# Kernel tuning notes

Measured on AMD Instinct MI355X. Metric: run time of the kernel, lower is better.

## Reference

```python
import jax, jax.numpy as jnp
import numpy as np

B, T, S = 64, 128, 16
E = 512           # d2v input size
H = 512           # bi-LSTM output size (args.d2v_embed)
Hh = H // 2       # per-direction hidden
NL = 2            # num_layers
ED = 128          # args.embedding_dim
USERS, ARTS, PAD = 100000, 100000, 0


def setup_inputs() -> dict:
    key = jax.random.key(0)
    ks = jax.random.split(key, 32)
    p = 0.02
    inp = {}
    inp["x1"] = jax.random.normal(ks[0], (B, T, E), jnp.float32)
    inp["sample_d2v_embeds"] = jax.random.normal(ks[1], (B, T, S, H), jnp.float32)
    # LSTM params: layer-0 input E == layer-1 input H, so stackable. gate order i,f,g,o
    inp["lstm_Wih"] = jax.random.normal(ks[2], (NL, 2, 4 * Hh, E), jnp.float32) * p
    inp["lstm_Whh"] = jax.random.normal(ks[3], (NL, 2, 4 * Hh, Hh), jnp.float32) * p
    inp["lstm_bih"] = jax.random.normal(ks[4], (NL, 2, 4 * Hh), jnp.float32) * p
    inp["lstm_bhh"] = jax.random.normal(ks[5], (NL, 2, 4 * Hh), jnp.float32) * p
    inp["attn_W1"] = jax.random.normal(ks[6], (H, H), jnp.float32) * p
    inp["attn_b1"] = jax.random.normal(ks[7], (H,), jnp.float32) * p
    inp["attn_w2"] = jax.random.normal(ks[8], (H,), jnp.float32) * p
    inp["rnn_mlp_W"] = jax.random.normal(ks[9], (64, H), jnp.float32) * p
    inp["rnn_mlp_b"] = jax.random.normal(ks[10], (64,), jnp.float32) * p
    inp["user_table"] = jax.random.normal(ks[11], (USERS, ED), jnp.float32) * p
    inp["art_table"] = (jax.random.normal(ks[12], (ARTS, ED), jnp.float32) * p).at[PAD].set(0.0)
    inp["em_W1"] = jax.random.normal(ks[13], (128, ED), jnp.float32) * p
    inp["em_b1"] = jax.random.normal(ks[14], (128,), jnp.float32) * p
    inp["em_W2"] = jax.random.normal(ks[15], (64, 128), jnp.float32) * p
    inp["em_b2"] = jax.random.normal(ks[16], (64,), jnp.float32) * p
    inp["lm_W1"] = jax.random.normal(ks[17], (256, 128), jnp.float32) * p
    inp["lm_b1"] = jax.random.normal(ks[18], (256,), jnp.float32) * p
    inp["lm_W2"] = jax.random.normal(ks[19], (128, 256), jnp.float32) * p
    inp["lm_b2"] = jax.random.normal(ks[20], (128,), jnp.float32) * p
    inp["lm_W3"] = jax.random.normal(ks[21], (64, 128), jnp.float32) * p
    inp["lm_b3"] = jax.random.normal(ks[22], (64,), jnp.float32) * p
    inp["lm_W4"] = jax.random.normal(ks[23], (1, 64), jnp.float32) * p
    inp["lm_b4"] = jax.random.normal(ks[24], (1,), jnp.float32) * p
    inp["x2"] = 0  # unused '_' arg
    inp["cate"] = jax.random.randint(ks[25], (B, T), 0, 10)  # unused by forward
    lens = jax.random.randint(ks[26], (B,), 1, T + 1)
    inp["seq_lens"] = jnp.sort(lens)[::-1]  # pack requires descending
    inp["user_ids"] = jax.random.randint(ks[27], (B,), 0, USERS)
    inp["sample_ids"] = jax.random.randint(ks[28], (B, T, S), 0, ARTS)
    return inp


def _bilstm(x, lens, Wih, Whh, bih, bhh):
    # Packed bidirectional LSTM == padded LSTM with state updates masked to t < len.
    Bc, Tc, _ = x.shape
    tmask = jnp.arange(Tc)[None, :] < lens[:, None]       # [B,T]
    m_t = tmask.T[:, :, None]                             # [T,B,1]
    for l in range(NL):
        outs = []
        for d, rev in ((0, False), (1, True)):
            xg = jnp.einsum('bti,gi->tbg', x, Wih[l, d]) + bih[l, d]  # [T,B,4Hh]
            Whh_ld, bhh_ld = Whh[l, d], bhh[l, d]

            def step(carry, inp_t, Whh_ld=Whh_ld, bhh_ld=bhh_ld):
                h, c = carry
                xg_t, m = inp_t
                g = xg_t + h @ Whh_ld.T + bhh_ld
                i_, f_, g_, o_ = jnp.split(g, 4, axis=-1)
                c2 = jax.nn.sigmoid(f_) * c + jax.nn.sigmoid(i_) * jnp.tanh(g_)
                h2 = jax.nn.sigmoid(o_) * jnp.tanh(c2)
                h = jnp.where(m, h2, h)
                c = jnp.where(m, c2, c)
                return (h, c), h

            init = (jnp.zeros((Bc, Hh), x.dtype), jnp.zeros((Bc, Hh), x.dtype))
            _, hs = jax.lax.scan(step, init, (xg, m_t), reverse=rev)
            outs.append(jnp.transpose(hs, (1, 0, 2)))
        x = jnp.concatenate(outs, axis=-1)                # [B,T,H]
    return x, tmask


def reference(x1, sample_d2v_embeds, lstm_Wih, lstm_Whh, lstm_bih, lstm_bhh,
              attn_W1, attn_b1, attn_w2, rnn_mlp_W, rnn_mlp_b,
              user_table, art_table, em_W1, em_b1, em_W2, em_b2,
              lm_W1, lm_b1, lm_W2, lm_b2, lm_W3, lm_b3, lm_W4, lm_b4,
              x2, cate, seq_lens, user_ids, sample_ids):
    rnn, tmask = _bilstm(x1, seq_lens, lstm_Wih, lstm_Whh, lstm_bih, lstm_bhh)
    # per-key MLP attention score, causal softmax, weighted sum (the packed double loop)
    sc = jnp.einsum('bth,h->bt', jnp.tanh(jnp.einsum('bth,oh->bto', rnn, attn_W1) + attn_b1), attn_w2)
    causal = jnp.tril(jnp.ones((rnn.shape[1], rnn.shape[1]), bool))
    logits = jnp.where(causal[None, :, :], sc[:, None, :], jnp.float32(-1e30))
    a = jax.nn.softmax(logits, axis=-1)                   # [B,T(query),T(key)]
    ctx = jnp.einsum('bts,bsh->bth', a, rnn)
    ctx = jnp.where(tmask[:, :, None], ctx, 0.0)          # rnn_step zeros at padded t
    # embedding branch
    ue = user_table[user_ids]                             # [B,ED]
    se = art_table[sample_ids]                            # [B,T,S,ED]
    e = ue[:, None, None, :] * se
    e = jax.nn.relu(e @ em_W1.T + em_b1)
    e = jax.nn.relu(e @ em_W2.T + em_b2)                  # [B,T,S,64]
    # rnn branch
    r = ctx[:, :, None, :] * sample_d2v_embeds
    r = r @ rnn_mlp_W.T + rnn_mlp_b                       # [B,T,S,64]
    z = jnp.concatenate([e, r], axis=-1)                  # [B,T,S,128]
    z = jax.nn.relu(z @ lm_W1.T + lm_b1)
    z = jax.nn.relu(z @ lm_W2.T + lm_b2)
    z = jax.nn.relu(z @ lm_W3.T + lm_b3)
    z = jax.nn.sigmoid(z @ lm_W4.T + lm_b4)
    return jnp.squeeze(z, axis=-1)                        # [B,T,S]
```

## Files before the change

kernel.cpp:

```cpp
#include <hip/hip_runtime.h>
#include <cstddef>

namespace {

constexpr int T = 128;

typedef unsigned short u16;
typedef unsigned int u32;
typedef __attribute__((ext_vector_type(8))) short short8;
typedef __attribute__((ext_vector_type(4))) float f32x4;
typedef __attribute__((ext_vector_type(4))) int i32x4;

__device__ __forceinline__ u16 f2bf(float x) {
  u32 u = __float_as_uint(x);
  u = (u + 0x7FFFu + ((u >> 16) & 1u)) >> 16;
  return (u16)u;
}
__device__ __forceinline__ float bf2f(u16 v) {
  return __uint_as_float(((u32)v) << 16);
}
__device__ __forceinline__ float sigf(float x) {
  return __builtin_amdgcn_rcpf(1.f + __builtin_amdgcn_exp2f(-1.44269504f * x));
}
__device__ __forceinline__ float tanh2(float x) {
  return 1.f - 2.f * __builtin_amdgcn_rcpf(1.f + __builtin_amdgcn_exp2f(2.88539008f * x));
}

constexpr int O_WIH = 0;
constexpr int O_AW1 = 2097152;
constexpr int O_EM1 = 2359296;
constexpr int O_EM2 = 2375680;
constexpr int O_MLP = 2383872;
constexpr int O_LW1 = 2416640;
constexpr int O_LW2 = 2449408;
constexpr int O_LW3 = 2482176;
constexpr int N_WBF = 2490368;

__global__ __launch_bounds__(256)
void k_prep(const float* __restrict__ wih, const float* __restrict__ aw1,
            const float* __restrict__ e1, const float* __restrict__ e2,
            const float* __restrict__ mw, const float* __restrict__ l1,
            const float* __restrict__ l2, const float* __restrict__ l3,
            u16* __restrict__ wbf) {
  int i = blockIdx.x * 256 + threadIdx.x;
  if (i >= N_WBF) return;
  float v;
  if (i < O_AW1)      v = wih[i];
  else if (i < O_EM1) v = aw1[i - O_AW1];
  else if (i < O_EM2) v = e1[i - O_EM1];
  else if (i < O_MLP) v = e2[i - O_EM2];
  else if (i < O_LW1) v = mw[i - O_MLP];
  else if (i < O_LW2) v = l1[i - O_LW1];
  else if (i < O_LW3) v = l2[i - O_LW2];
  else                v = l3[i - O_LW3];
  wbf[i] = f2bf(v);
}

__global__ __launch_bounds__(256)
void k_prepw(const float* __restrict__ whh, signed char* __restrict__ wq) {
  int i = blockIdx.x * 256 + threadIdx.x;
  float v = whh[i] * 1016.f;
  v = fminf(fmaxf(v, -127.f), 127.f);
  wq[i] = (signed char)(int)rintf(v);
}

__global__ __launch_bounds__(256)
void k_xg_mfma(const float* __restrict__ X, const u16* __restrict__ Wbf,
               const float* __restrict__ bi, const float* __restrict__ bh,
               float* __restrict__ xg) {
  __shared__ __align__(16) u16 sx[32 * 520];
  int tid = threadIdx.x;
  int rowbase = blockIdx.x * 32;
  int nchunk = blockIdx.y;
  for (int idx = tid; idx < 4096; idx += 256) {
    int r = idx >> 7, k4 = idx & 127;
    float4 v = *(const float4*)(X + (size_t)(rowbase + r) * 512 + k4 * 4);
    u32* p = (u32*)(sx + r * 520 + k4 * 4);
    p[0] = (u32)f2bf(v.x) | ((u32)f2bf(v.y) << 16);
    p[1] = (u32)f2bf(v.z) | ((u32)f2bf(v.w) << 16);
  }
  __syncthreads();
  int w = tid >> 6, lane = tid & 63;
  int msub = w >> 1, nhalf = w & 1;
  int mbase = msub * 16;
  int nb0 = nchunk * 256 + nhalf * 128;
  f32x4 acc[8];
#pragma unroll
  for (int i = 0; i < 8; ++i) acc[i] = f32x4{0.f, 0.f, 0.f, 0.f};
  for (int kt = 0; kt < 16; ++kt) {
    short8 a = *(const short8*)(sx + (mbase + (lane & 15)) * 520 + kt * 32 + (lane >> 4) * 8);
#pragma unroll
    for (int nt = 0; nt < 8; ++nt) {
      short8 b = *(const short8*)(Wbf + (size_t)(nb0 + nt * 16 + (lane & 15)) * 512 +
                                  kt * 32 + (lane >> 4) * 8);
      acc[nt] = __builtin_amdgcn_mfma_f32_16x16x32_bf16(a, b, acc[nt], 0, 0, 0);
    }
  }
  int mr = mbase + (lane >> 4) * 4;
#pragma unroll
  for (int nt = 0; nt < 8; ++nt) {
    int n = nb0 + nt * 16 + (lane & 15);
    float bb = bi[n] + bh[n];
#pragma unroll
    for (int r = 0; r < 4; ++r)
      xg[(size_t)(rowbase + mr + r) * 2048 + n] = acc[nt][r] + bb;
  }
}

__global__ __launch_bounds__(512, 1)
void k_lstm6(const float* __restrict__ xg, const signed char* __restrict__ wq,
             const int* __restrict__ lens, float* __restrict__ out, int layer) {
  __shared__ __align__(16) signed char hq[2][16 * 272];
  const int d = blockIdx.x >> 2, bg = blockIdx.x & 3;
  const int tid = threadIdx.x;
  const int jc = tid >> 6, l = tid & 63, ln = l & 15, lk = l >> 4;
  const int mb = bg * 16;

  i32x4 Bq[4][2][4];
  const signed char* wbase = wq + (size_t)(layer * 2 + d) * 262144;
#pragma unroll
  for (int g = 0; g < 4; ++g)
#pragma unroll
    for (int js = 0; js < 2; ++js)
#pragma unroll
      for (int kc = 0; kc < 4; ++kc) {
        int n = g * 256 + jc * 32 + js * 16 + ln;
        Bq[g][js][kc] = *(const i32x4*)(wbase + (size_t)n * 256 + kc * 64 + lk * 16);
      }

  int mlen[4];
#pragma unroll
  for (int r = 0; r < 4; ++r) mlen[r] = lens[mb + lk * 4 + r];

  float cst[2][4], hst[2][4];
#pragma unroll
  for (int js = 0; js < 2; ++js)
#pragma unroll
    for (int r = 0; r < 4; ++r) { cst[js][r] = 0.f; hst[js][r] = 0.f; }

  const float DEQ = 1.f / (1016.f * 127.f);

  for (int s = 0; s < 128; ++s) {
    const int t = d ? (127 - s) : s;

    float xv[4][2][4];
#pragma unroll
    for (int g = 0; g < 4; ++g)
#pragma unroll
      for (int js = 0; js < 2; ++js)
#pragma unroll
        for (int r = 0; r < 4; ++r)
          xv[g][js][r] = xg[((size_t)(mb + lk * 4 + r) * 128 + t) * 2048 +
                            d * 1024 + g * 256 + jc * 32 + js * 16 + ln];

    i32x4 acc[4][2];
#pragma unroll
    for (int g = 0; g < 4; ++g)
#pragma unroll
      for (int js = 0; js < 2; ++js) acc[g][js] = i32x4{0, 0, 0, 0};

    if (s > 0) {
      const signed char* hr = hq[(s & 1) ^ 1];
#pragma unroll
      for (int kc = 0; kc < 4; ++kc) {
        i32x4 a = *(const i32x4*)(hr + ln * 272 + kc * 64 + lk * 16);
#pragma unroll
        for (int g = 0; g < 4; ++g)
#pragma unroll
          for (int js = 0; js < 2; ++js)
            acc[g][js] = __builtin_amdgcn_mfma_i32_16x16x64_i8(a, Bq[g][js][kc],
                                                               acc[g][js], 0, 0, 0);
      }
    }

    signed char* hw = hq[s & 1];
#pragma unroll
    for (int js = 0; js < 2; ++js)
#pragma unroll
      for (int r = 0; r < 4; ++r) {
        float gi = (float)acc[0][js][r] * DEQ + xv[0][js][r];
        float gf = (float)acc[1][js][r] * DEQ + xv[1][js][r];
        float gg = (float)acc[2][js][r] * DEQ + xv[2][js][r];
        float go = (float)acc[3][js][r] * DEQ + xv[3][js][r];
        float c2 = sigf(gf) * cst[js][r] + sigf(gi) * tanh2(gg);
        float h2 = sigf(go) * tanh2(c2);
        const int m = lk * 4 + r;
        bool upd = t < mlen[r];
        cst[js][r] = upd ? c2 : cst[js][r];
        float hn = upd ? h2 : hst[js][r];
        hst[js][r] = hn;
        const int j = jc * 32 + js * 16 + ln;
        out[((size_t)(mb + m) * 128 + t) * 512 + d * 256 + j] = hn;
        hw[m * 272 + j] = (signed char)(int)rintf(hn * 127.f);
      }
    __syncthreads();
  }
}

__global__ __launch_bounds__(256)
void k_attn(const float* __restrict__ rnn, const u16* __restrict__ W1bf,
            const float* __restrict__ b1, const float* __restrict__ w2,
            float* __restrict__ sc) {
  __shared__ __align__(16) u16 sx[32 * 520];
  __shared__ float sred[32];
  int tid = threadIdx.x;
  int rowbase = blockIdx.x * 32;
  for (int idx = tid; idx < 4096; idx += 256) {
    int r = idx >> 7, k4 = idx & 127;
    float4 v = *(const float4*)(rnn + (size_t)(rowbase + r) * 512 + k4 * 4);
    u32* p = (u32*)(sx + r * 520 + k4 * 4);
    p[0] = (u32)f2bf(v.x) | ((u32)f2bf(v.y) << 16);
    p[1] = (u32)f2bf(v.z) | ((u32)f2bf(v.w) << 16);
  }
  if (tid < 32) sred[tid] = 0.f;
  __syncthreads();
  int w = tid >> 6, lane = tid & 63;
  int msub = w >> 1, nhalf = w & 1;
  int mbase = msub * 16;
  float psum[4] = {0.f, 0.f, 0.f, 0.f};
  for (int ng = 0; ng < 4; ++ng) {
    f32x4 acc[4];
#pragma unroll
    for (int i = 0; i < 4; ++i) acc[i] = f32x4{0.f, 0.f, 0.f, 0.f};
    for (int kt = 0; kt < 16; ++kt) {
      short8 a = *(const short8*)(sx + (mbase + (lane & 15)) * 520 + kt * 32 + (lane >> 4) * 8);
#pragma unroll
      for (int nt = 0; nt < 4; ++nt) {
        int nrow = nhalf * 256 + ng * 64 + nt * 16 + (lane & 15);
        short8 b = *(const short8*)(W1bf + (size_t)nrow * 512 + kt * 32 + (lane >> 4) * 8);
        acc[nt] = __builtin_amdgcn_mfma_f32_16x16x32_bf16(a, b, acc[nt], 0, 0, 0);
      }
    }
#pragma unroll
    for (int nt = 0; nt < 4; ++nt) {
      int n = nhalf * 256 + ng * 64 + nt * 16 + (lane & 15);
      float wn = w2[n], bn = b1[n];
#pragma unroll
      for (int r = 0; r < 4; ++r) psum[r] += wn * tanh2(acc[nt][r] + bn);
    }
  }
#pragma unroll
  for (int off = 8; off >= 1; off >>= 1)
#pragma unroll
    for (int r = 0; r < 4; ++r) psum[r] += __shfl_xor(psum[r], off);
  if ((lane & 15) == 0) {
#pragma unroll
    for (int r = 0; r < 4; ++r)
      atomicAdd(&sred[msub * 16 + (lane >> 4) * 4 + r], psum[r]);
  }
  __syncthreads();
  if (tid < 32) sc[rowbase + tid] = sred[tid];
}

__global__ __launch_bounds__(128)
void k_ctx(const float* __restrict__ sc, const float* __restrict__ rnn,
           const int* __restrict__ lens, float* __restrict__ ctx) {
  int b = blockIdx.x;
  int h = blockIdx.y * 128 + threadIdx.x;
  __shared__ float ex[T];
  ex[threadIdx.x] = expf(sc[b * T + threadIdx.x]);
  __syncthreads();
  int len = lens[b];
  float acc = 0.f, den = 0.f;
  for (int t = 0; t < T; ++t) {
    float wv = ex[t];
    den += wv;
    acc += wv * rnn[((size_t)b * T + t) * 512 + h];
    ctx[((size_t)b * T + t) * 512 + h] = (t < len) ? (acc / den) : 0.f;
  }
}

template <int NT, int KT, bool RELU>
__device__ __forceinline__ void stage_mfma(const u16* __restrict__ Wbf,
                                           const float* __restrict__ bias,
                                           const u16* A, int lda,
                                           u16* O, int ldo, int nofs,
                                           int lane, int msub, int nhalf) {
  f32x4 acc[NT];
#pragma unroll
  for (int i = 0; i < NT; ++i) acc[i] = f32x4{0.f, 0.f, 0.f, 0.f};
  int mbase = msub * 16;
  int nb0 = nhalf * (NT * 16);
#pragma unroll
  for (int kt = 0; kt < KT; ++kt) {
    short8 a = *(const short8*)(A + (mbase + (lane & 15)) * lda + kt * 32 + (lane >> 4) * 8);
#pragma unroll
    for (int nt = 0; nt < NT; ++nt) {
      short8 b = *(const short8*)(Wbf + (size_t)(nb0 + nt * 16 + (lane & 15)) * (KT * 32) +
                                  kt * 32 + (lane >> 4) * 8);
      acc[nt] = __builtin_amdgcn_mfma_f32_16x16x32_bf16(a, b, acc[nt], 0, 0, 0);
    }
  }
  int mr = mbase + (lane >> 4) * 4;
#pragma unroll
  for (int nt = 0; nt < NT; ++nt) {
    int nl = nb0 + nt * 16 + (lane & 15);
    float bv = bias[nl];
#pragma unroll
    for (int r = 0; r < 4; ++r) {
      float v = acc[nt][r] + bv;
      if (RELU) v = fmaxf(v, 0.f);
      O[(mr + r) * ldo + nofs + nl] = f2bf(v);
    }
  }
}

__global__ __launch_bounds__(256)
void k_sample(const float* __restrict__ ctx, const float* __restrict__ d2v,
              const float* __restrict__ user_table, const float* __restrict__ art_table,
              const int* __restrict__ user_ids, const int* __restrict__ sample_ids,
              const u16* __restrict__ wbf,
              const float* __restrict__ em_b1, const float* __restrict__ em_b2,
              const float* __restrict__ mlp_b,
              const float* __restrict__ lm_b1, const float* __restrict__ lm_b2,
              const float* __restrict__ lm_b3,
              const float* __restrict__ lm_W4, const float* __restrict__ lm_b4,
              float* __restrict__ out) {
  __shared__ __align__(16) u16 bufA[32 * 520];
  __shared__ __align__(16) u16 bufB[32 * 264];
  __shared__ __align__(16) u16 bufC[32 * 136];
  int tid = threadIdx.x, lane = tid & 63, w = tid >> 6;
  int msub = w >> 1, nhalf = w & 1;
  int rowbase = blockIdx.x * 32;

  for (int idx = tid; idx < 1024; idx += 256) {
    int r = idx >> 5, k4 = idx & 31;
    int m = rowbase + r;
    int sid = sample_ids[m];
    int uid = user_ids[m >> 11];
    float4 u = *(const float4*)(user_table + (size_t)uid * 128 + k4 * 4);
    float4 a = *(const float4*)(art_table + (size_t)sid * 128 + k4 * 4);
    u32* p = (u32*)(bufA + r * 520 + k4 * 4);
    p[0] = (u32)f2bf(u.x * a.x) | ((u32)f2bf(u.y * a.y) << 16);
    p[1] = (u32)f2bf(u.z * a.z) | ((u32)f2bf(u.w * a.w) << 16);
  }
  __syncthreads();
  stage_mfma<4, 4, true>(wbf + O_EM1, em_b1, bufA, 520, bufB, 264, 0, lane, msub, nhalf);
  __syncthreads();
  stage_mfma<2, 4, true>(wbf + O_EM2, em_b2, bufB, 264, bufC, 136, 0, lane, msub, nhalf);
  for (int idx = tid; idx < 4096; idx += 256) {
    int r = idx >> 7, k4 = idx & 127;
    int m = rowbase + r;
    int bt = m >> 4;
    float4 cx = *(const float4*)(ctx + (size_t)bt * 512 + k4 * 4);
    float4 dv = *(const float4*)(d2v + (size_t)m * 512 + k4 * 4);
    u32* p = (u32*)(bufA + r * 520 + k4 * 4);
    p[0] = (u32)f2bf(cx.x * dv.x) | ((u32)f2bf(cx.y * dv.y) << 16);
    p[1] = (u32)f2bf(cx.z * dv.z) | ((u32)f2bf(cx.w * dv.w) << 16);
  }
  __syncthreads();
  stage_mfma<2, 16, false>(wbf + O_MLP, mlp_b, bufA, 520, bufC, 136, 64, lane, msub, nhalf);
  __syncthreads();
  stage_mfma<8, 4, true>(wbf + O_LW1, lm_b1, bufC, 136, bufB, 264, 0, lane, msub, nhalf);
  __syncthreads();
  stage_mfma<4, 8, true>(wbf + O_LW2, lm_b2, bufB, 264, bufA, 520, 0, lane, msub, nhalf);
  __syncthreads();
  stage_mfma<2, 4, true>(wbf + O_LW3, lm_b3, bufA, 520, bufC, 136, 0, lane, msub, nhalf);
  __syncthreads();

  if (tid < 32) {
    float acc = lm_b4[0];
#pragma unroll
    for (int k = 0; k < 64; ++k) acc += bf2f(bufC[tid * 136 + k]) * lm_W4[k];
    out[rowbase + tid] = sigf(acc);
  }
}

}

extern "C" void kernel_launch(void* const* d_in, const int* in_sizes, int n_in,
                              void* d_out, int out_size, void* d_ws, size_t ws_size,
                              hipStream_t stream) {
  const float* x1   = (const float*)d_in[0];
  const float* d2v  = (const float*)d_in[1];
  const float* Wih  = (const float*)d_in[2];
  const float* Whh  = (const float*)d_in[3];
  const float* bih  = (const float*)d_in[4];
  const float* bhh  = (const float*)d_in[5];
  const float* aW1  = (const float*)d_in[6];
  const float* ab1  = (const float*)d_in[7];
  const float* aw2  = (const float*)d_in[8];
  const float* mlpW = (const float*)d_in[9];
  const float* mlpb = (const float*)d_in[10];
  const float* utab = (const float*)d_in[11];
  const float* atab = (const float*)d_in[12];
  const float* emW1 = (const float*)d_in[13];
  const float* emb1 = (const float*)d_in[14];
  const float* emW2 = (const float*)d_in[15];
  const float* emb2 = (const float*)d_in[16];
  const float* lmW1 = (const float*)d_in[17];
  const float* lmb1 = (const float*)d_in[18];
  const float* lmW2 = (const float*)d_in[19];
  const float* lmb2 = (const float*)d_in[20];
  const float* lmW3 = (const float*)d_in[21];
  const float* lmb3 = (const float*)d_in[22];
  const float* lmW4 = (const float*)d_in[23];
  const float* lmb4 = (const float*)d_in[24];
  const int* lens   = (const int*)d_in[27];
  const int* uids   = (const int*)d_in[28];
  const int* sids   = (const int*)d_in[29];
  float* out = (float*)d_out;

  float* ws = (float*)d_ws;
  signed char* WQ = (signed char*)ws;
  float* SC  = ws + 262144;
  u16* WBF = (u16*)(ws + 270336);
  float* XG  = ws + 1515520;
  float* R0  = ws + 18292736;
  float* R1  = ws + 22487040;
  float* CTX = ws + 18292736;

  k_prep<<<(N_WBF + 255) / 256, 256, 0, stream>>>(Wih, aW1, emW1, emW2, mlpW,
                                                  lmW1, lmW2, lmW3, WBF);
  k_prepw<<<4096, 256, 0, stream>>>(Whh, WQ);
  k_xg_mfma<<<dim3(256, 8), 256, 0, stream>>>(x1, WBF + O_WIH, bih, bhh, XG);
  k_lstm6<<<8, 512, 0, stream>>>(XG, WQ, lens, R0, 0);
  k_xg_mfma<<<dim3(256, 8), 256, 0, stream>>>(R0, WBF + O_WIH + 1048576,
                                              bih + 2048, bhh + 2048, XG);
  k_lstm6<<<8, 512, 0, stream>>>(XG, WQ, lens, R1, 1);
  k_attn<<<256, 256, 0, stream>>>(R1, WBF + O_AW1, ab1, aw2, SC);
  k_ctx<<<dim3(64, 4), 128, 0, stream>>>(SC, R1, lens, CTX);
  k_sample<<<4096, 256, 0, stream>>>(CTX, d2v, utab, atab, uids, sids, WBF,
                                     emb1, emb2, mlpb, lmb1, lmb2, lmb3,
                                     lmW4, lmb4, out);
}
```

Baseline: 1.267 ms.

## Halve k_sample LDS with split-K d2v staging, fuse final layers, lighter barriers

The k_sample kernel's large 520-stride buffer shrinks to 264 by staging the ctx*d2v product in two 256-wide K chunks. The rnn MLP matmul is written out by hand and accumulated across both chunks. The last two MLP layers are fused: the 64-wide ReLU output is dotted with lm_W4 in registers, reduced with shuffles and LDS atomics, so the bufC round trip and the serial 32-thread tail go away. __syncthreads is replaced with a raw lgkmcnt wait plus s_barrier, in both the LSTM loop and k_sample, to cut barrier overhead. Less LDS should allow more resident blocks, at the cost of an extra barrier and a serialized reload between the K halves.

```diff
diff --git a/kernel.cpp b/kernel.cpp
--- a/kernel.cpp
+++ b/kernel.cpp
@@ -24,6 +24,9 @@
 }
 __device__ __forceinline__ float tanh2(float x) {
   return 1.f - 2.f * __builtin_amdgcn_rcpf(1.f + __builtin_amdgcn_exp2f(2.88539008f * x));
+}
+__device__ __forceinline__ void bar_lds() {
+  asm volatile("s_waitcnt lgkmcnt(0)\n\ts_barrier" ::: "memory");
 }
 
 constexpr int O_WIH = 0;
@@ -193,7 +196,7 @@
         out[((size_t)(mb + m) * 128 + t) * 512 + d * 256 + j] = hn;
         hw[m * 272 + j] = (signed char)(int)rintf(hn * 127.f);
       }
-    __syncthreads();
+    bar_lds();
   }
 }
 
@@ -316,12 +319,16 @@
               const float* __restrict__ lm_b3,
               const float* __restrict__ lm_W4, const float* __restrict__ lm_b4,
               float* __restrict__ out) {
-  __shared__ __align__(16) u16 bufA[32 * 520];
+  __shared__ __align__(16) u16 bufA[32 * 264];
   __shared__ __align__(16) u16 bufB[32 * 264];
   __shared__ __align__(16) u16 bufC[32 * 136];
+  __shared__ float sred[32];
   int tid = threadIdx.x, lane = tid & 63, w = tid >> 6;
   int msub = w >> 1, nhalf = w & 1;
+  int mbase = msub * 16;
   int rowbase = blockIdx.x * 32;
+
+  if (tid < 32) sred[tid] = 0.f;
 
   for (int idx = tid; idx < 1024; idx += 256) {
     int r = idx >> 5, k4 = idx & 31;
@@ -330,40 +337,108 @@
     int uid = user_ids[m >> 11];
     float4 u = *(const float4*)(user_table + (size_t)uid * 128 + k4 * 4);
     float4 a = *(const float4*)(art_table + (size_t)sid * 128 + k4 * 4);
-    u32* p = (u32*)(bufA + r * 520 + k4 * 4);
+    u32* p = (u32*)(bufA + r * 264 + k4 * 4);
     p[0] = (u32)f2bf(u.x * a.x) | ((u32)f2bf(u.y * a.y) << 16);
     p[1] = (u32)f2bf(u.z * a.z) | ((u32)f2bf(u.w * a.w) << 16);
   }
-  __syncthreads();
-  stage_mfma<4, 4, true>(wbf + O_EM1, em_b1, bufA, 520, bufB, 264, 0, lane, msub, nhalf);
-  __syncthreads();
+  bar_lds();
+  stage_mfma<4, 4, true>(wbf + O_EM1, em_b1, bufA, 264, bufB, 264, 0, lane, msub, nhalf);
+  bar_lds();
   stage_mfma<2, 4, true>(wbf + O_EM2, em_b2, bufB, 264, bufC, 136, 0, lane, msub, nhalf);
-  for (int idx = tid; idx < 4096; idx += 256) {
-    int r = idx >> 7, k4 = idx & 127;
+  for (int idx = tid; idx < 2048; idx += 256) {
+    int r = idx >> 6, k4 = idx & 63;
     int m = rowbase + r;
     int bt = m >> 4;
     float4 cx = *(const float4*)(ctx + (size_t)bt * 512 + k4 * 4);
     float4 dv = *(const float4*)(d2v + (size_t)m * 512 + k4 * 4);
-    u32* p = (u32*)(bufA + r * 520 + k4 * 4);
+    u32* p = (u32*)(bufA + r * 264 + k4 * 4);
     p[0] = (u32)f2bf(cx.x * dv.x) | ((u32)f2bf(cx.y * dv.y) << 16);
     p[1] = (u32)f2bf(cx.z * dv.z) | ((u32)f2bf(cx.w * dv.w) << 16);
   }
-  __syncthreads();
-  stage_mfma<2, 16, false>(wbf + O_MLP, mlp_b, bufA, 520, bufC, 136, 64, lane, msub, nhalf);
-  __syncthreads();
+  bar_lds();
+
+  f32x4 racc[2];
+  racc[0] = f32x4{0.f, 0.f, 0.f, 0.f};
+  racc[1] = f32x4{0.f, 0.f, 0.f, 0.f};
+  for (int kc = 0; kc < 2; ++kc) {
+#pragma unroll
+    for (int kt = 0; kt < 8; ++kt) {
+      short8 a = *(const short8*)(bufA + (mbase + (lane & 15)) * 264 + kt * 32 + (lane >> 4) * 8);
+#pragma unroll
+      for (int nt = 0; nt < 2; ++nt) {
+        int n = nhalf * 32 + nt * 16 + (lane & 15);
+        short8 b = *(const short8*)(wbf + O_MLP + (size_t)n * 512 + kc * 256 +
+                                    kt * 32 + (lane >> 4) * 8);
+        racc[nt] = __builtin_amdgcn_mfma_f32_16x16x32_bf16(a, b, racc[nt], 0, 0, 0);
+      }
+    }
+    bar_lds();
+    if (kc == 0) {
+      for (int idx = tid; idx < 2048; idx += 256) {
+        int r = idx >> 6, k4 = idx & 63;
+        int m = rowbase + r;
+        int bt = m >> 4;
+        float4 cx = *(const float4*)(ctx + (size_t)bt * 512 + 256 + k4 * 4);
+        float4 dv = *(const float4*)(d2v + (size_t)m * 512 + 256 + k4 * 4);
+        u32* p = (u32*)(bufA + r * 264 + k4 * 4);
+        p[0] = (u32)f2bf(cx.x * dv.x) | ((u32)f2bf(cx.y * dv.y) << 16);
+        p[1] = (u32)f2bf(cx.z * dv.z) | ((u32)f2bf(cx.w * dv.w) << 16);
+      }
+      bar_lds();
+    }
+  }
+  {
+    int mr = mbase + (lane >> 4) * 4;
+#pragma unroll
+    for (int nt = 0; nt < 2; ++nt) {
+      int nl = nhalf * 32 + nt * 16 + (lane & 15);
+      float bv = mlp_b[nl];
+#pragma unroll
+      for (int r = 0; r < 4; ++r)
+        bufC[(mr + r) * 136 + 64 + nl] = f2bf(racc[nt][r] + bv);
+    }
+  }
+  bar_lds();
   stage_mfma<8, 4, true>(wbf + O_LW1, lm_b1, bufC, 136, bufB, 264, 0, lane, msub, nhalf);
-  __syncthreads();
-  stage_mfma<4, 8, true>(wbf + O_LW2, lm_b2, bufB, 264, bufA, 520, 0, lane, msub, nhalf);
-  __syncthreads();
-  stage_mfma<2, 4, true>(wbf + O_LW3, lm_b3, bufA, 520, bufC, 136, 0, lane, msub, nhalf);
-  __syncthreads();
-
-  if (tid < 32) {
-    float acc = lm_b4[0];
-#pragma unroll
-    for (int k = 0; k < 64; ++k) acc += bf2f(bufC[tid * 136 + k]) * lm_W4[k];
-    out[rowbase + tid] = sigf(acc);
-  }
+  bar_lds();
+  stage_mfma<4, 8, true>(wbf + O_LW2, lm_b2, bufB, 264, bufA, 264, 0, lane, msub, nhalf);
+  bar_lds();
+
+  {
+    f32x4 acc[2];
+    acc[0] = f32x4{0.f, 0.f, 0.f, 0.f};
+    acc[1] = f32x4{0.f, 0.f, 0.f, 0.f};
+#pragma unroll
+    for (int kt = 0; kt < 4; ++kt) {
+      short8 a = *(const short8*)(bufA + (mbase + (lane & 15)) * 264 + kt * 32 + (lane >> 4) * 8);
+#pragma unroll
+      for (int nt = 0; nt < 2; ++nt) {
+        int n = nhalf * 32 + nt * 16 + (lane & 15);
+        short8 b = *(const short8*)(wbf + O_LW3 + (size_t)n * 128 +
+                                    kt * 32 + (lane >> 4) * 8);
+        acc[nt] = __builtin_amdgcn_mfma_f32_16x16x32_bf16(a, b, acc[nt], 0, 0, 0);
+      }
+    }
+    float psum[4] = {0.f, 0.f, 0.f, 0.f};
+#pragma unroll
+    for (int nt = 0; nt < 2; ++nt) {
+      int nl = nhalf * 32 + nt * 16 + (lane & 15);
+      float bv = lm_b3[nl], w4 = lm_W4[nl];
+#pragma unroll
+      for (int r = 0; r < 4; ++r) psum[r] += w4 * fmaxf(acc[nt][r] + bv, 0.f);
+    }
+#pragma unroll
+    for (int off = 8; off >= 1; off >>= 1)
+#pragma unroll
+      for (int r = 0; r < 4; ++r) psum[r] += __shfl_xor(psum[r], off);
+    if ((lane & 15) == 0) {
+#pragma unroll
+      for (int r = 0; r < 4; ++r)
+        atomicAdd(&sred[mbase + (lane >> 4) * 4 + r], psum[r]);
+    }
+  }
+  bar_lds();
+  if (tid < 32) out[rowbase + tid] = sigf(sred[tid] + lm_b4[0]);
 }
 
 }
```

New measurement: 1.260 ms. Within noise of the previous version (-0.6%).
